# Optimization experiments

Measured on AMD Instinct MI355X. Metric: run time of the kernel, lower is better.

Reference implementation:

```python
import jax, jax.numpy as jnp
import numpy as np

# Predictive-coding graph message passing (PCGraphConv core compute).
# Single-graph edge list (edge_src -> edge_dst) with one scalar weight per edge,
# tiled over the batch (weights.repeat(1, batchsize) in the original).
# PredictionMessagePassing: mu_i = sum_{e: dst(e)=i} w_e * f(x_{src(e)})
# ValueMessagePassing:      dx_j = -eps_j + f'(x_j) * sum_{e: src(e)=j} w_e * eps_{dst(e)}
# with eps = x - mu and f = tanh.

N_PER_GRAPH = 4096
E_PER_GRAPH = 524288
BATCH = 32


def setup_inputs() -> dict:
    key = jax.random.key(0)
    k1, k2, k3, k4 = jax.random.split(key, 4)
    x = jax.random.normal(k1, (BATCH * N_PER_GRAPH,), dtype=jnp.float32)
    weights = jax.random.normal(k2, (E_PER_GRAPH,), dtype=jnp.float32) * (1.0 / np.sqrt(N_PER_GRAPH))
    edge_src = jax.random.randint(k3, (E_PER_GRAPH,), 0, N_PER_GRAPH, dtype=jnp.int32)
    edge_dst = jax.random.randint(k4, (E_PER_GRAPH,), 0, N_PER_GRAPH, dtype=jnp.int32)
    return {"x": x, "weights": weights, "edge_src": edge_src, "edge_dst": edge_dst,
            "batch_size": BATCH, "num_vertices": N_PER_GRAPH}


def reference(x, weights, edge_src, edge_dst, batch_size, num_vertices):
    B, N = batch_size, num_vertices
    BN = B * N
    # Tile single-graph edges across the batch with per-graph node offsets.
    offs = (jnp.arange(B, dtype=edge_src.dtype) * N)[:, None]        # [B,1]
    src = (edge_src[None, :] + offs).reshape(-1)                     # [B*E]
    dst = (edge_dst[None, :] + offs).reshape(-1)                     # [B*E]
    w = jnp.tile(weights, B)                                         # [B*E]

    fx = jnp.tanh(x)                                                 # f(x)
    # Predictions: gather f(x) at src, weight per edge, scatter-add at dst.
    mu = jax.ops.segment_sum(w * fx[src], dst, num_segments=BN)      # [B*N]
    eps = x - mu                                                     # errors
    fprime = 1.0 - fx * fx                                           # f'(x)
    # Value update: backward flow of errors along edges.
    dx = -eps + fprime * jax.ops.segment_sum(w * eps[dst], src, num_segments=BN)
    return jnp.stack([mu, dx])                                       # [2, B*N]
```

## Files before the change

kernel.cpp:

```cpp
#include <hip/hip_runtime.h>


static constexpr int kB = 32, kLogB = 5;
static constexpr int kBkt = 256;
static constexpr int kNPB = 16;
static constexpr int kChunk = 2048;
static constexpr int kTile = 2560;

__global__ void __launch_bounds__(1024) k_hist(
    const int* __restrict__ esrc, const int* __restrict__ edst,
    const float* __restrict__ x, float* __restrict__ x_t,
    float* __restrict__ fx_t, unsigned* __restrict__ cntA,
    unsigned* __restrict__ cntB, int N, int E, int nBB) {
  __shared__ unsigned hA[kBkt], hB[kBkt];
  __shared__ float tile[32][65];
  int tid = threadIdx.x, blk = blockIdx.x;
  if (blk < nBB) {
    if (tid < kBkt) { hA[tid] = 0u; hB[tid] = 0u; }
    __syncthreads();
    int e0 = blk * kChunk, len = min(kChunk, E - e0);
    for (int i = tid; i < len; i += 1024) {
      atomicAdd(&hA[((unsigned)edst[e0 + i]) >> 4], 1u);
      atomicAdd(&hB[((unsigned)esrc[e0 + i]) >> 4], 1u);
    }
    __syncthreads();
    if (tid < kBkt) {
      cntA[(size_t)blk * kBkt + tid] = hA[tid];
      cntB[(size_t)blk * kBkt + tid] = hB[tid];
    }
  } else if (blk - nBB < (N >> 6)) {
    int n0 = (blk - nBB) * 64;
    for (int k = tid; k < 32 * 64; k += 1024) {
      int b = k >> 6, n = k & 63;
      tile[b][n] = x[b * N + n0 + n];
    }
    __syncthreads();
    for (int k = tid; k < 64 * 32; k += 1024) {
      int n = k >> 5, b = k & 31;
      float xv = tile[b][n];
      int j = (n0 + n) * kB + b;
      x_t[j] = xv;
      fx_t[j] = tanhf(xv);
    }
  }
}

__global__ void __launch_bounds__(1024) k_scan(
    const unsigned* __restrict__ cntA, const unsigned* __restrict__ cntB,
    unsigned* __restrict__ baseA, unsigned* __restrict__ baseB,
    unsigned* __restrict__ segA, unsigned* __restrict__ segB, int nBB) {
  __shared__ unsigned qoff[4][kBkt];
  __shared__ unsigned tot[kBkt];
  __shared__ unsigned bb[kBkt];
  const unsigned* cnt = blockIdx.x ? cntB : cntA;
  unsigned* base = blockIdx.x ? baseB : baseA;
  unsigned* seg  = blockIdx.x ? segB  : segA;
  int tid = threadIdx.x;
  int t = tid & (kBkt - 1), q = tid >> 8;
  int qlen = (nBB + 3) >> 2;
  int b0 = q * qlen;
  unsigned run = 0;
  for (int j = 0; j < qlen; j += 8) {
    unsigned c[8];
#pragma unroll
    for (int u = 0; u < 8; ++u) {
      int bi = b0 + j + u;
      c[u] = (bi < nBB) ? cnt[(size_t)bi * kBkt + t] : 0u;
    }
#pragma unroll
    for (int u = 0; u < 8; ++u) run += c[u];
  }
  qoff[q][t] = run;
  __syncthreads();
  unsigned myTot = 0;
  if (tid < kBkt) {
    unsigned p0 = qoff[0][tid], p1 = qoff[1][tid];
    unsigned p2 = qoff[2][tid], p3 = qoff[3][tid];
    qoff[0][tid] = 0u; qoff[1][tid] = p0;
    qoff[2][tid] = p0 + p1; qoff[3][tid] = p0 + p1 + p2;
    myTot = p0 + p1 + p2 + p3;
    tot[tid] = myTot;
  }
  __syncthreads();
  for (int o = 1; o < kBkt; o <<= 1) {
    unsigned v = 0;
    if (tid < kBkt && tid >= o) v = tot[tid - o];
    __syncthreads();
    if (tid < kBkt && tid >= o) tot[tid] += v;
    __syncthreads();
  }
  if (tid < kBkt) {
    unsigned excl = tot[tid] - myTot;
    bb[tid] = excl;
    seg[tid] = excl;
    if (tid == kBkt - 1) seg[kBkt] = excl + myTot;
  }
  __syncthreads();
  run = bb[t] + qoff[q][t];
  for (int j = 0; j < qlen; j += 8) {
    unsigned c[8];
#pragma unroll
    for (int u = 0; u < 8; ++u) {
      int bi = b0 + j + u;
      c[u] = (bi < nBB) ? cnt[(size_t)bi * kBkt + t] : 0u;
    }
#pragma unroll
    for (int u = 0; u < 8; ++u) {
      int bi = b0 + j + u;
      if (bi < nBB) base[(size_t)bi * kBkt + t] = run;
      run += c[u];
    }
  }
}

__global__ void __launch_bounds__(1024) k_scatter(
    const int* __restrict__ esrc, const int* __restrict__ edst,
    const float* __restrict__ wgt,
    const unsigned* __restrict__ cntA, const unsigned* __restrict__ cntB,
    const unsigned* __restrict__ baseA, const unsigned* __restrict__ baseB,
    uint2* __restrict__ recA, uint2* __restrict__ recB, int E, int nBB) {
  __shared__ unsigned myBase[kBkt], cntL[kBkt], baseL[kBkt], cnt2[kBkt];
  __shared__ uint2 cmp[kChunk];
  __shared__ unsigned char bktid[kChunk];
  int tid = threadIdx.x, blk = blockIdx.x;
  int e0 = blk * kChunk, len = min(kChunk, E - e0);
  for (int dir = 0; dir < 2; ++dir) {
    const int* key = dir ? esrc : edst;
    const int* oth = dir ? edst : esrc;
    const unsigned* cnt = dir ? cntB : cntA;
    const unsigned* base = dir ? baseB : baseA;
    uint2* out = dir ? recB : recA;
    if (tid < kBkt) {
      myBase[tid] = base[(size_t)blk * kBkt + tid];
      cntL[tid] = cnt[(size_t)blk * kBkt + tid];
      cnt2[tid] = 0u;
    }
    __syncthreads();
    if (tid < 64) {
      int qq = tid << 2;
      unsigned c0 = cntL[qq], c1 = cntL[qq + 1];
      unsigned c2 = cntL[qq + 2], c3 = cntL[qq + 3];
      unsigned s = c0 + c1 + c2 + c3, run = s;
#pragma unroll
      for (int o = 1; o < 64; o <<= 1) {
        unsigned v = __shfl_up(run, o, 64);
        if (tid >= o) run += v;
      }
      unsigned bse = run - s;
      baseL[qq] = bse; baseL[qq + 1] = bse + c0;
      baseL[qq + 2] = bse + c0 + c1; baseL[qq + 3] = bse + c0 + c1 + c2;
    }
    __syncthreads();
    for (int i = tid; i < len; i += 1024) {
      unsigned ky = (unsigned)key[e0 + i], ot = (unsigned)oth[e0 + i];
      unsigned bbk = ky >> 4;
      unsigned slot = baseL[bbk] + atomicAdd(&cnt2[bbk], 1u);
      cmp[slot] = make_uint2((ot << 4) | (ky & 15u), __float_as_uint(wgt[e0 + i]));
      bktid[slot] = (unsigned char)bbk;
    }
    __syncthreads();
    for (int s = tid; s < len; s += 1024) {
      unsigned bbk = bktid[s];
      out[myBase[bbk] + ((unsigned)s - baseL[bbk])] = cmp[s];
    }
    __syncthreads();
  }
}

__global__ void __launch_bounds__(1024) k_pass(
    const uint2* __restrict__ rec, const unsigned* __restrict__ seg,
    const float* __restrict__ vals, const float* __restrict__ x_t,
    const float* __restrict__ fx_t, float* __restrict__ eps_t,
    float* __restrict__ out, int N, int mode) {
  __shared__ uint2 srt[kTile];
  __shared__ unsigned hW[16 * kNPB];
  __shared__ unsigned wbase[16 * kNPB];
  __shared__ unsigned wcur[16 * kNPB];
  __shared__ unsigned h[kNPB], hb[kNPB];
  __shared__ float red[1024];
  int tid = threadIdx.x, t = blockIdx.x;
  int segb = (int)seg[t], sege = (int)seg[t + 1];
  int wv = tid >> 6;
  int b = tid & 31, hw = tid >> 5, l = hw >> 1, part = hw & 1;
  float acc = 0.0f;

  for (int t0 = segb; t0 < sege; t0 += kTile) {
    int len = min(kTile, sege - t0);
    if (tid < 16 * kNPB) { hW[tid] = 0u; wcur[tid] = 0u; }
    __syncthreads();
    for (int i = tid; i < len; i += 1024)
      atomicAdd(&hW[wv * kNPB + (rec[t0 + i].x & 15u)], 1u);
    __syncthreads();
    if (tid < kNPB) {
      unsigned run = 0;
#pragma unroll
      for (int w2 = 0; w2 < 16; ++w2) {
        unsigned c = hW[w2 * kNPB + tid];
        wbase[w2 * kNPB + tid] = run;
        run += c;
      }
      h[tid] = run;
    }
    __syncthreads();
    if (tid == 0) {
      unsigned run = 0;
#pragma unroll
      for (int l2 = 0; l2 < kNPB; ++l2) { hb[l2] = run; run += h[l2]; }
    }
    __syncthreads();
    if (tid < 16 * kNPB) wbase[tid] += hb[tid & (kNPB - 1)];
    __syncthreads();
    for (int i = tid; i < len; i += 1024) {
      uint2 r = rec[t0 + i];
      unsigned lx = r.x & 15u;
      srt[wbase[wv * kNPB + lx] + atomicAdd(&wcur[wv * kNPB + lx], 1u)] = r;
    }
    __syncthreads();

    int beg = (int)hb[l] + part, end = (int)hb[l] + (int)h[l];
    int last = end - 1; if (last < 0) last = 0;
    uint2 r0, r1, r2, r3, r4, r5, r6, r7;
    float v0, v1, v2, v3, v4, v5, v6, v7;
#define PC_LOAD(d)                                                   \
    { int p = beg + 2 * (d); uint2 rr = srt[min(p, last)];           \
      r##d = rr; v##d = vals[(((rr.x >> 4) & 4095u) << kLogB) + b]; }
    PC_LOAD(0) PC_LOAD(1) PC_LOAD(2) PC_LOAD(3)
    PC_LOAD(4) PC_LOAD(5) PC_LOAD(6) PC_LOAD(7)
#undef PC_LOAD
    int i = beg;
    while (i < end) {
#define PC_STEP(d)                                                   \
      { float wt = (i + 2 * (d) < end) ? __uint_as_float(r##d.y) : 0.0f; \
        acc = fmaf(wt, v##d, acc);                                   \
        int p = i + 16 + 2 * (d); uint2 rr = srt[min(p, last)];      \
        r##d = rr; v##d = vals[(((rr.x >> 4) & 4095u) << kLogB) + b]; }
      PC_STEP(0) PC_STEP(1) PC_STEP(2) PC_STEP(3)
      PC_STEP(4) PC_STEP(5) PC_STEP(6) PC_STEP(7)
#undef PC_STEP
      i += 16;
    }
    __syncthreads();
  }

  red[tid] = acc;
  __syncthreads();
  if (part == 0) {
    float s = red[tid] + red[tid + 32];
    int n = t * kNPB + l;
    int j = (n << kLogB) + b;
    if (mode == 0) {
      out[b * N + n] = s;
      eps_t[j] = x_t[j] - s;
    } else {
      float fx = fx_t[j];
      out[b * N + n] = fmaf(1.0f - fx * fx, s, -eps_t[j]);
    }
  }
}

extern "C" void kernel_launch(void* const* d_in, const int* in_sizes, int n_in,
                              void* d_out, int out_size, void* d_ws, size_t ws_size,
                              hipStream_t stream) {
  const float* x    = (const float*)d_in[0];
  const float* w    = (const float*)d_in[1];
  const int*   esrc = (const int*)d_in[2];
  const int*   edst = (const int*)d_in[3];

  int BN = in_sizes[0];
  int E  = in_sizes[1];
  int N  = BN / kB;
  int nBB = (E + kChunk - 1) / kChunk;

  float* ws    = (float*)d_ws;
  float* x_t   = ws;
  float* fx_t  = ws + (size_t)BN;
  float* eps_t = ws + 2 * (size_t)BN;
  unsigned* cntA = (unsigned*)(ws + 3 * (size_t)BN);
  unsigned* cntB = cntA + (size_t)nBB * kBkt;
  unsigned* baseA = cntB + (size_t)nBB * kBkt;
  unsigned* baseB = baseA + (size_t)nBB * kBkt;
  unsigned* segA = baseB + (size_t)nBB * kBkt;
  unsigned* segB = segA + 512;
  uint2* recA = (uint2*)(segB + 512);
  uint2* recB = recA + (size_t)E;

  float* out_mu = (float*)d_out;
  float* out_dx = (float*)d_out + BN;

  k_hist<<<nBB + (N >> 6), 1024, 0, stream>>>(esrc, edst, x, x_t, fx_t,
                                              cntA, cntB, N, E, nBB);
  k_scan<<<2, 1024, 0, stream>>>(cntA, cntB, baseA, baseB, segA, segB, nBB);
  k_scatter<<<nBB, 1024, 0, stream>>>(esrc, edst, w, cntA, cntB, baseA, baseB,
                                      recA, recB, E, nBB);
  k_pass<<<kBkt, 1024, 0, stream>>>(recA, segA, fx_t, x_t, fx_t,
                                    eps_t, out_mu, N, 0);
  k_pass<<<kBkt, 1024, 0, stream>>>(recB, segB, eps_t, x_t, fx_t,
                                    eps_t, out_dx, N, 1);
}
```

Measured before the change: 107.5 us.

## Fuse bucket scan into scatter kernel and split directions across blocks

Removes the separate 2-block scan kernel by having every scatter block redundantly recompute its column prefix and global segment offsets from the count matrix. The scatter grid doubles so each block handles a single direction instead of looping over both. In the pass kernel, each tile of records is staged into shared memory once so the sort step does not reread global memory. The trade-off is redundant reads of the whole 256x256 count matrix per block (512 blocks) and extra LDS use in k_pass.

```diff
diff --git a/kernel.cpp b/kernel.cpp
--- a/kernel.cpp
+++ b/kernel.cpp
@@ -45,125 +45,105 @@
   }
 }
 
-__global__ void __launch_bounds__(1024) k_scan(
-    const unsigned* __restrict__ cntA, const unsigned* __restrict__ cntB,
-    unsigned* __restrict__ baseA, unsigned* __restrict__ baseB,
-    unsigned* __restrict__ segA, unsigned* __restrict__ segB, int nBB) {
-  __shared__ unsigned qoff[4][kBkt];
-  __shared__ unsigned tot[kBkt];
-  __shared__ unsigned bb[kBkt];
-  const unsigned* cnt = blockIdx.x ? cntB : cntA;
-  unsigned* base = blockIdx.x ? baseB : baseA;
-  unsigned* seg  = blockIdx.x ? segB  : segA;
-  int tid = threadIdx.x;
-  int t = tid & (kBkt - 1), q = tid >> 8;
-  int qlen = (nBB + 3) >> 2;
-  int b0 = q * qlen;
-  unsigned run = 0;
-  for (int j = 0; j < qlen; j += 8) {
-    unsigned c[8];
-#pragma unroll
-    for (int u = 0; u < 8; ++u) {
-      int bi = b0 + j + u;
-      c[u] = (bi < nBB) ? cnt[(size_t)bi * kBkt + t] : 0u;
-    }
-#pragma unroll
-    for (int u = 0; u < 8; ++u) run += c[u];
-  }
-  qoff[q][t] = run;
-  __syncthreads();
-  unsigned myTot = 0;
-  if (tid < kBkt) {
-    unsigned p0 = qoff[0][tid], p1 = qoff[1][tid];
-    unsigned p2 = qoff[2][tid], p3 = qoff[3][tid];
-    qoff[0][tid] = 0u; qoff[1][tid] = p0;
-    qoff[2][tid] = p0 + p1; qoff[3][tid] = p0 + p1 + p2;
-    myTot = p0 + p1 + p2 + p3;
-    tot[tid] = myTot;
-  }
-  __syncthreads();
-  for (int o = 1; o < kBkt; o <<= 1) {
-    unsigned v = 0;
-    if (tid < kBkt && tid >= o) v = tot[tid - o];
-    __syncthreads();
-    if (tid < kBkt && tid >= o) tot[tid] += v;
-    __syncthreads();
-  }
-  if (tid < kBkt) {
-    unsigned excl = tot[tid] - myTot;
-    bb[tid] = excl;
-    seg[tid] = excl;
-    if (tid == kBkt - 1) seg[kBkt] = excl + myTot;
-  }
-  __syncthreads();
-  run = bb[t] + qoff[q][t];
-  for (int j = 0; j < qlen; j += 8) {
-    unsigned c[8];
-#pragma unroll
-    for (int u = 0; u < 8; ++u) {
-      int bi = b0 + j + u;
-      c[u] = (bi < nBB) ? cnt[(size_t)bi * kBkt + t] : 0u;
-    }
-#pragma unroll
-    for (int u = 0; u < 8; ++u) {
-      int bi = b0 + j + u;
-      if (bi < nBB) base[(size_t)bi * kBkt + t] = run;
-      run += c[u];
-    }
-  }
-}
-
 __global__ void __launch_bounds__(1024) k_scatter(
     const int* __restrict__ esrc, const int* __restrict__ edst,
     const float* __restrict__ wgt,
     const unsigned* __restrict__ cntA, const unsigned* __restrict__ cntB,
-    const unsigned* __restrict__ baseA, const unsigned* __restrict__ baseB,
-    uint2* __restrict__ recA, uint2* __restrict__ recB, int E, int nBB) {
+    uint2* __restrict__ recA, uint2* __restrict__ recB,
+    unsigned* __restrict__ segA, unsigned* __restrict__ segB,
+    int E, int nBB) {
+  __shared__ unsigned qpre[4][kBkt], qtot[4][kBkt];
+  __shared__ unsigned colPre[kBkt], colTot[kBkt], segL[kBkt];
   __shared__ unsigned myBase[kBkt], cntL[kBkt], baseL[kBkt], cnt2[kBkt];
   __shared__ uint2 cmp[kChunk];
   __shared__ unsigned char bktid[kChunk];
   int tid = threadIdx.x, blk = blockIdx.x;
-  int e0 = blk * kChunk, len = min(kChunk, E - e0);
-  for (int dir = 0; dir < 2; ++dir) {
-    const int* key = dir ? esrc : edst;
-    const int* oth = dir ? edst : esrc;
-    const unsigned* cnt = dir ? cntB : cntA;
-    const unsigned* base = dir ? baseB : baseA;
-    uint2* out = dir ? recB : recA;
-    if (tid < kBkt) {
-      myBase[tid] = base[(size_t)blk * kBkt + tid];
-      cntL[tid] = cnt[(size_t)blk * kBkt + tid];
-      cnt2[tid] = 0u;
-    }
-    __syncthreads();
-    if (tid < 64) {
-      int qq = tid << 2;
-      unsigned c0 = cntL[qq], c1 = cntL[qq + 1];
-      unsigned c2 = cntL[qq + 2], c3 = cntL[qq + 3];
-      unsigned s = c0 + c1 + c2 + c3, run = s;
-#pragma unroll
-      for (int o = 1; o < 64; o <<= 1) {
-        unsigned v = __shfl_up(run, o, 64);
-        if (tid >= o) run += v;
-      }
-      unsigned bse = run - s;
-      baseL[qq] = bse; baseL[qq + 1] = bse + c0;
-      baseL[qq + 2] = bse + c0 + c1; baseL[qq + 3] = bse + c0 + c1 + c2;
-    }
-    __syncthreads();
-    for (int i = tid; i < len; i += 1024) {
-      unsigned ky = (unsigned)key[e0 + i], ot = (unsigned)oth[e0 + i];
-      unsigned bbk = ky >> 4;
-      unsigned slot = baseL[bbk] + atomicAdd(&cnt2[bbk], 1u);
-      cmp[slot] = make_uint2((ot << 4) | (ky & 15u), __float_as_uint(wgt[e0 + i]));
-      bktid[slot] = (unsigned char)bbk;
-    }
-    __syncthreads();
-    for (int s = tid; s < len; s += 1024) {
-      unsigned bbk = bktid[s];
-      out[myBase[bbk] + ((unsigned)s - baseL[bbk])] = cmp[s];
-    }
-    __syncthreads();
+  int dir = (blk >= nBB);
+  int c = blk - (dir ? nBB : 0);
+  const unsigned* cnt = dir ? cntB : cntA;
+  uint2* out = dir ? recB : recA;
+
+  int t = tid & (kBkt - 1), q = tid >> 8;
+  int qlen = (nBB + 3) >> 2;
+  int r0 = q * qlen;
+  unsigned pre = 0, tot = 0;
+  for (int j = 0; j < qlen; j += 8) {
+    unsigned cc[8];
+#pragma unroll
+    for (int u = 0; u < 8; ++u) {
+      int row = r0 + j + u;
+      cc[u] = (row < nBB) ? cnt[(size_t)row * kBkt + t] : 0u;
+    }
+#pragma unroll
+    for (int u = 0; u < 8; ++u) {
+      int row = r0 + j + u;
+      tot += cc[u];
+      if (row < c) pre += cc[u];
+    }
+  }
+  qpre[q][t] = pre;
+  qtot[q][t] = tot;
+  __syncthreads();
+  if (tid < kBkt) {
+    colPre[tid] = qpre[0][tid] + qpre[1][tid] + qpre[2][tid] + qpre[3][tid];
+    colTot[tid] = qtot[0][tid] + qtot[1][tid] + qtot[2][tid] + qtot[3][tid];
+  }
+  __syncthreads();
+  if (tid < 64) {
+    int qq = tid << 2;
+    unsigned c0 = colTot[qq], c1 = colTot[qq + 1];
+    unsigned c2 = colTot[qq + 2], c3 = colTot[qq + 3];
+    unsigned s = c0 + c1 + c2 + c3, run = s;
+#pragma unroll
+    for (int o = 1; o < 64; o <<= 1) {
+      unsigned v = __shfl_up(run, o, 64);
+      if (tid >= o) run += v;
+    }
+    unsigned bse = run - s;
+    segL[qq] = bse; segL[qq + 1] = bse + c0;
+    segL[qq + 2] = bse + c0 + c1; segL[qq + 3] = bse + c0 + c1 + c2;
+  }
+  __syncthreads();
+  if (c == 0 && tid < kBkt) {
+    unsigned* seg = dir ? segB : segA;
+    seg[tid] = segL[tid];
+    if (tid == kBkt - 1) seg[kBkt] = segL[tid] + colTot[tid];
+  }
+  if (tid < kBkt) {
+    myBase[tid] = segL[tid] + colPre[tid];
+    cntL[tid] = cnt[(size_t)c * kBkt + tid];
+    cnt2[tid] = 0u;
+  }
+  __syncthreads();
+  if (tid < 64) {
+    int qq = tid << 2;
+    unsigned c0 = cntL[qq], c1 = cntL[qq + 1];
+    unsigned c2 = cntL[qq + 2], c3 = cntL[qq + 3];
+    unsigned s = c0 + c1 + c2 + c3, run = s;
+#pragma unroll
+    for (int o = 1; o < 64; o <<= 1) {
+      unsigned v = __shfl_up(run, o, 64);
+      if (tid >= o) run += v;
+    }
+    unsigned bse = run - s;
+    baseL[qq] = bse; baseL[qq + 1] = bse + c0;
+    baseL[qq + 2] = bse + c0 + c1; baseL[qq + 3] = bse + c0 + c1 + c2;
+  }
+  __syncthreads();
+  int e0 = c * kChunk, len = min(kChunk, E - e0);
+  const int* key = dir ? esrc : edst;
+  const int* oth = dir ? edst : esrc;
+  for (int i = tid; i < len; i += 1024) {
+    unsigned ky = (unsigned)key[e0 + i], ot = (unsigned)oth[e0 + i];
+    unsigned bbk = ky >> 4;
+    unsigned slot = baseL[bbk] + atomicAdd(&cnt2[bbk], 1u);
+    cmp[slot] = make_uint2((ot << 4) | (ky & 15u), __float_as_uint(wgt[e0 + i]));
+    bktid[slot] = (unsigned char)bbk;
+  }
+  __syncthreads();
+  for (int s = tid; s < len; s += 1024) {
+    unsigned bbk = bktid[s];
+    out[myBase[bbk] + ((unsigned)s - baseL[bbk])] = cmp[s];
   }
 }
 
@@ -172,6 +152,7 @@
     const float* __restrict__ vals, const float* __restrict__ x_t,
     const float* __restrict__ fx_t, float* __restrict__ eps_t,
     float* __restrict__ out, int N, int mode) {
+  __shared__ uint2 stg[kTile];
   __shared__ uint2 srt[kTile];
   __shared__ unsigned hW[16 * kNPB];
   __shared__ unsigned wbase[16 * kNPB];
@@ -188,8 +169,11 @@
     int len = min(kTile, sege - t0);
     if (tid < 16 * kNPB) { hW[tid] = 0u; wcur[tid] = 0u; }
     __syncthreads();
-    for (int i = tid; i < len; i += 1024)
-      atomicAdd(&hW[wv * kNPB + (rec[t0 + i].x & 15u)], 1u);
+    for (int i = tid; i < len; i += 1024) {
+      uint2 r = rec[t0 + i];
+      stg[i] = r;
+      atomicAdd(&hW[wv * kNPB + (r.x & 15u)], 1u);
+    }
     __syncthreads();
     if (tid < kNPB) {
       unsigned run = 0;
@@ -211,7 +195,7 @@
     if (tid < 16 * kNPB) wbase[tid] += hb[tid & (kNPB - 1)];
     __syncthreads();
     for (int i = tid; i < len; i += 1024) {
-      uint2 r = rec[t0 + i];
+      uint2 r = stg[i];
       unsigned lx = r.x & 15u;
       srt[wbase[wv * kNPB + lx] + atomicAdd(&wcur[wv * kNPB + lx], 1u)] = r;
     }
@@ -277,9 +261,7 @@
   float* eps_t = ws + 2 * (size_t)BN;
   unsigned* cntA = (unsigned*)(ws + 3 * (size_t)BN);
   unsigned* cntB = cntA + (size_t)nBB * kBkt;
-  unsigned* baseA = cntB + (size_t)nBB * kBkt;
-  unsigned* baseB = baseA + (size_t)nBB * kBkt;
-  unsigned* segA = baseB + (size_t)nBB * kBkt;
+  unsigned* segA = cntB + (size_t)nBB * kBkt;
   unsigned* segB = segA + 512;
   uint2* recA = (uint2*)(segB + 512);
   uint2* recB = recA + (size_t)E;
@@ -289,9 +271,8 @@
 
   k_hist<<<nBB + (N >> 6), 1024, 0, stream>>>(esrc, edst, x, x_t, fx_t,
                                               cntA, cntB, N, E, nBB);
-  k_scan<<<2, 1024, 0, stream>>>(cntA, cntB, baseA, baseB, segA, segB, nBB);
-  k_scatter<<<nBB, 1024, 0, stream>>>(esrc, edst, w, cntA, cntB, baseA, baseB,
-                                      recA, recB, E, nBB);
+  k_scatter<<<2 * nBB, 1024, 0, stream>>>(esrc, edst, w, cntA, cntB,
+                                          recA, recB, segA, segB, E, nBB);
   k_pass<<<kBkt, 1024, 0, stream>>>(recA, segA, fx_t, x_t, fx_t,
                                     eps_t, out_mu, N, 0);
   k_pass<<<kBkt, 1024, 0, stream>>>(recB, segB, eps_t, x_t, fx_t,
```

Result: faster. 101.9 us (-5.2%).
